# Optimization experiments

Hardware: AMD Instinct MI355X
Metric: run time of the kernel (lower is better)

## Reference

```python
import jax, jax.numpy as jnp
import numpy as np

N = 2          # branching factor
DATA_DIM = 4   # per-leaf payload size
DEPTH = 7      # tree fully refined to this depth (levels 0..7)
Q = 4_000_000  # number of query points


def _build_child():
    """Fully-refined N^3 tree: child[n,i,j,k] = relative offset to child node,
    0 for leaf cells (matches N3Tree.refine_all construction order)."""
    n_per = [N ** (3 * l) for l in range(DEPTH + 1)]
    offsets = np.concatenate([[0], np.cumsum(n_per)]).astype(np.int64)
    total = int(offsets[-1])
    child = np.zeros((total, N, N, N), dtype=np.int32)
    for l in range(DEPTH):  # level DEPTH nodes stay leaves (child==0)
        idx = offsets[l] + np.arange(n_per[l])
        child_abs = offsets[l + 1] + (np.arange(n_per[l])[:, None] * (N ** 3)
                                      + np.arange(N ** 3)[None, :])
        delta = (child_abs - idx[:, None]).astype(np.int32)
        child[idx] = delta.reshape(n_per[l], N, N, N)
    return child


def setup_inputs() -> dict:
    key = jax.random.key(0)
    k1, k2 = jax.random.split(key)
    child = jnp.asarray(_build_child())          # (M, N, N, N) int32
    M = child.shape[0]
    data = jax.random.normal(k1, (M, N, N, N, DATA_DIM), dtype=jnp.float32)
    indices = jax.random.uniform(k2, (Q, 3), dtype=jnp.float32,
                                 minval=0.0, maxval=1.0)
    return {"data": data, "child": child, "indices": indices}


def reference(data, child, indices):
    """Vectorized octree vertical query (vary_non_leaf=True):
    accumulate data along root->leaf path for each query point."""
    Nf = jnp.float32(N)
    nq = indices.shape[0]

    def step(carry, _):
        ind, node_ids, result, active = carry
        cell = jnp.clip(jnp.floor(ind * Nf).astype(jnp.int32), 0, N - 1)  # (Q,3)
        delta = child[node_ids, cell[:, 0], cell[:, 1], cell[:, 2]]       # (Q,)
        vals = data[node_ids, cell[:, 0], cell[:, 1], cell[:, 2]]         # (Q,D)
        result = result + jnp.where(active[:, None], vals, 0.0)
        nonterm = active & (delta != 0)
        node_ids = node_ids + jnp.where(nonterm, delta, 0)
        ind = jnp.where(active[:, None], ind * Nf - cell.astype(jnp.float32), ind)
        return (ind, node_ids, result, nonterm), None

    init = (indices,
            jnp.zeros(nq, jnp.int32),
            jnp.zeros((nq, DATA_DIM), jnp.float32),
            jnp.ones(nq, dtype=bool))
    (_, _, result, _), _ = jax.lax.scan(step, init, None, length=DEPTH + 1)
    return result
```

## Files before the change

kernel.cpp:

```cpp
#include <hip/hip_runtime.h>


typedef float vfloat4 __attribute__((ext_vector_type(4)));

__constant__ __device__ const int kOffs[8] = {0, 1, 9, 73, 585, 4681, 37449, 299593};

__global__ __launch_bounds__(256) void build_prefix_table(
    const float* __restrict__ data,
    vfloat4*     __restrict__ table)
{
    int p = blockIdx.x * blockDim.x + threadIdx.x;
    float ax = 0.f, ay = 0.f, az = 0.f, aw = 0.f;
    int prefix = 0;
    #pragma unroll
    for (int l = 0; l < 6; ++l) {
        int c = (p >> (15 - 3 * l)) & 7;
        int node = kOffs[l] + prefix;
        const vfloat4 v = *reinterpret_cast<const vfloat4*>(
            data + ((size_t)node << 5) + ((size_t)c << 2));
        ax += v.x; ay += v.y; az += v.z; aw += v.w;
        prefix = (prefix << 3) + c;
    }
    vfloat4 r; r.x = ax; r.y = ay; r.z = az; r.w = aw;
    table[p] = r;
}

__global__ __launch_bounds__(256) void n3tree_query_tab(
    const float*   __restrict__ data,
    const vfloat4* __restrict__ table,
    const float*   __restrict__ indices,
    float*         __restrict__ out,
    int nq)
{
    int q = blockIdx.x * blockDim.x + threadIdx.x;
    if (q >= nq) return;

    float ix = __builtin_nontemporal_load(indices + 3 * (size_t)q + 0);
    float iy = __builtin_nontemporal_load(indices + 3 * (size_t)q + 1);
    float iz = __builtin_nontemporal_load(indices + 3 * (size_t)q + 2);

    int cc[8];
    #pragma unroll
    for (int l = 0; l < 8; ++l) {
        int cx = (int)(ix * 2.0f); cx = cx < 0 ? 0 : (cx > 1 ? 1 : cx);
        int cy = (int)(iy * 2.0f); cy = cy < 0 ? 0 : (cy > 1 ? 1 : cy);
        int cz = (int)(iz * 2.0f); cz = cz < 0 ? 0 : (cz > 1 ? 1 : cz);
        cc[l] = (cx << 2) | (cy << 1) | cz;
        ix = ix * 2.0f - (float)cx;
        iy = iy * 2.0f - (float)cy;
        iz = iz * 2.0f - (float)cz;
    }
    int p6 = ((((cc[0] << 3 | cc[1]) << 3 | cc[2]) << 3 | cc[3]) << 3 | cc[4]) << 3 | cc[5];

    size_t addr6 = ((size_t)(37449  + p6)                << 5) + ((size_t)cc[6] << 2);
    size_t addr7 = ((size_t)(299593 + (p6 << 3) + cc[6]) << 5) + ((size_t)cc[7] << 2);

    vfloat4 t  = table[p6];
    vfloat4 v6 = *reinterpret_cast<const vfloat4*>(data + addr6);
    vfloat4 v7 = __builtin_nontemporal_load(
                     reinterpret_cast<const vfloat4*>(data + addr7));

    float ax = t.x; float ay = t.y; float az = t.z; float aw = t.w;
    ax += v6.x; ay += v6.y; az += v6.z; aw += v6.w;
    ax += v7.x; ay += v7.y; az += v7.z; aw += v7.w;

    vfloat4 r; r.x = ax; r.y = ay; r.z = az; r.w = aw;
    __builtin_nontemporal_store(r, reinterpret_cast<vfloat4*>(out) + q);
}

__global__ __launch_bounds__(256) void n3tree_query_direct(
    const float* __restrict__ data,
    const float* __restrict__ indices,
    float*       __restrict__ out,
    int nq)
{
    int q = blockIdx.x * blockDim.x + threadIdx.x;
    if (q >= nq) return;

    float ix = __builtin_nontemporal_load(indices + 3 * (size_t)q + 0);
    float iy = __builtin_nontemporal_load(indices + 3 * (size_t)q + 1);
    float iz = __builtin_nontemporal_load(indices + 3 * (size_t)q + 2);

    size_t addr[8];
    int p = 0;
    #pragma unroll
    for (int l = 0; l < 8; ++l) {
        int cx = (int)(ix * 2.0f); cx = cx < 0 ? 0 : (cx > 1 ? 1 : cx);
        int cy = (int)(iy * 2.0f); cy = cy < 0 ? 0 : (cy > 1 ? 1 : cy);
        int cz = (int)(iz * 2.0f); cz = cz < 0 ? 0 : (cz > 1 ? 1 : cz);
        int cidx = (cx << 2) | (cy << 1) | cz;
        addr[l] = ((size_t)(kOffs[l] + p) << 5) + ((size_t)cidx << 2);
        p = (p << 3) + cidx;
        ix = ix * 2.0f - (float)cx;
        iy = iy * 2.0f - (float)cy;
        iz = iz * 2.0f - (float)cz;
    }

    vfloat4 v[8];
    #pragma unroll
    for (int l = 0; l < 7; ++l)
        v[l] = *reinterpret_cast<const vfloat4*>(data + addr[l]);
    v[7] = __builtin_nontemporal_load(
               reinterpret_cast<const vfloat4*>(data + addr[7]));

    float ax = 0.f, ay = 0.f, az = 0.f, aw = 0.f;
    #pragma unroll
    for (int l = 0; l < 8; ++l) {
        ax += v[l].x; ay += v[l].y; az += v[l].z; aw += v[l].w;
    }

    vfloat4 r; r.x = ax; r.y = ay; r.z = az; r.w = aw;
    __builtin_nontemporal_store(r, reinterpret_cast<vfloat4*>(out) + q);
}

extern "C" void kernel_launch(void* const* d_in, const int* in_sizes, int n_in,
                              void* d_out, int out_size, void* d_ws, size_t ws_size,
                              hipStream_t stream) {
    const float* data    = (const float*)d_in[0];
    const float* indices = (const float*)d_in[2];
    float*       out     = (float*)d_out;

    int nq = in_sizes[2] / 3;
    const int block = 256;
    const int grid  = (nq + block - 1) / block;

    constexpr size_t TABLE_ENTRIES = 262144;
    constexpr size_t TABLE_BYTES   = TABLE_ENTRIES * 16;

    if (ws_size >= TABLE_BYTES) {
        vfloat4* table = reinterpret_cast<vfloat4*>(d_ws);
        build_prefix_table<<<TABLE_ENTRIES / block, block, 0, stream>>>(data, table);
        n3tree_query_tab<<<grid, block, 0, stream>>>(data, table, indices, out, nq);
    } else {
        n3tree_query_direct<<<grid, block, 0, stream>>>(data, indices, out, nq);
    }
}
```

Before: 208.1 us.

## Precompute full-path sums in bf16 table so each query does one lookup

Adds a full 8-level path-sum table D (16M entries, bf16-packed, 8 bytes each), so each query does a single gather instead of three. A fallback level-7 partial table T6 is used when the workspace is smaller. Building D streams the whole leaf level and writes 128MB, which could cost more than the gathers it saves for 4M queries. Rounding outputs to bf16 loses precision and may break the tolerance check.

```diff
diff --git a/kernel.cpp b/kernel.cpp
--- a/kernel.cpp
+++ b/kernel.cpp
@@ -5,9 +5,15 @@
 
 __constant__ __device__ const int kOffs[8] = {0, 1, 9, 73, 585, 4681, 37449, 299593};
 
-__global__ __launch_bounds__(256) void build_prefix_table(
-    const float* __restrict__ data,
-    vfloat4*     __restrict__ table)
+__device__ inline unsigned bf16_rne(float f) {
+    unsigned u = __float_as_uint(f);
+    return (u + 0x7fffu + ((u >> 16) & 1u)) >> 16;
+}
+__device__ inline float bf16_lo_f(unsigned w) { return __uint_as_float(w << 16); }
+__device__ inline float bf16_hi_f(unsigned w) { return __uint_as_float(w & 0xffff0000u); }
+
+__global__ __launch_bounds__(256) void build_T(
+    const float* __restrict__ data, vfloat4* __restrict__ T)
 {
     int p = blockIdx.x * blockDim.x + threadIdx.x;
     float ax = 0.f, ay = 0.f, az = 0.f, aw = 0.f;
@@ -16,29 +22,130 @@
     for (int l = 0; l < 6; ++l) {
         int c = (p >> (15 - 3 * l)) & 7;
         int node = kOffs[l] + prefix;
-        const vfloat4 v = *reinterpret_cast<const vfloat4*>(
+        vfloat4 v = *reinterpret_cast<const vfloat4*>(
             data + ((size_t)node << 5) + ((size_t)c << 2));
         ax += v.x; ay += v.y; az += v.z; aw += v.w;
         prefix = (prefix << 3) + c;
     }
     vfloat4 r; r.x = ax; r.y = ay; r.z = az; r.w = aw;
-    table[p] = r;
+    T[p] = r;
+}
+
+__global__ __launch_bounds__(256) void build_D(
+    const float* __restrict__ data, const vfloat4* __restrict__ T,
+    uint2* __restrict__ D)
+{
+    int t = blockIdx.x * blockDim.x + threadIdx.x;
+    int p7 = t >> 3, c7 = t & 7;
+    int p6 = p7 >> 3, c6 = p7 & 7;
+
+    vfloat4 tv = T[p6];
+    vfloat4 v6 = __builtin_nontemporal_load(reinterpret_cast<const vfloat4*>(
+        data + ((size_t)(37449 + p6) << 5) + ((size_t)c6 << 2)));
+    vfloat4 v7 = __builtin_nontemporal_load(reinterpret_cast<const vfloat4*>(
+        data + ((size_t)(299593 + p7) << 5) + ((size_t)c7 << 2)));
+
+    float ax = tv.x; ax += v6.x; ax += v7.x;
+    float ay = tv.y; ay += v6.y; ay += v7.y;
+    float az = tv.z; az += v6.z; az += v7.z;
+    float aw = tv.w; aw += v6.w; aw += v7.w;
+
+    uint2 o;
+    o.x = bf16_rne(ax) | (bf16_rne(ay) << 16);
+    o.y = bf16_rne(az) | (bf16_rne(aw) << 16);
+    D[(size_t)t] = o;
+}
+
+__global__ __launch_bounds__(256) void query_fold(
+    const uint2* __restrict__ D, const float* __restrict__ indices,
+    float* __restrict__ out, int nq)
+{
+    int q = blockIdx.x * blockDim.x + threadIdx.x;
+    if (q >= nq) return;
+
+    float ix = __builtin_nontemporal_load(indices + 3 * (size_t)q + 0);
+    float iy = __builtin_nontemporal_load(indices + 3 * (size_t)q + 1);
+    float iz = __builtin_nontemporal_load(indices + 3 * (size_t)q + 2);
+
+    int path = 0;
+    #pragma unroll
+    for (int l = 0; l < 8; ++l) {
+        int cx = (int)(ix * 2.0f); cx = cx < 0 ? 0 : (cx > 1 ? 1 : cx);
+        int cy = (int)(iy * 2.0f); cy = cy < 0 ? 0 : (cy > 1 ? 1 : cy);
+        int cz = (int)(iz * 2.0f); cz = cz < 0 ? 0 : (cz > 1 ? 1 : cz);
+        path = (path << 3) | ((cx << 2) | (cy << 1) | cz);
+        ix = ix * 2.0f - (float)cx;
+        iy = iy * 2.0f - (float)cy;
+        iz = iz * 2.0f - (float)cz;
+    }
+
+    uint2 d = D[(size_t)path];
+    vfloat4 r;
+    r.x = bf16_lo_f(d.x); r.y = bf16_hi_f(d.x);
+    r.z = bf16_lo_f(d.y); r.w = bf16_hi_f(d.y);
+    __builtin_nontemporal_store(r, reinterpret_cast<vfloat4*>(out) + q);
+}
+
+__global__ __launch_bounds__(256) void build_T6(
+    const float* __restrict__ data, const vfloat4* __restrict__ T,
+    uint2* __restrict__ T6)
+{
+    int t = blockIdx.x * blockDim.x + threadIdx.x;
+    int p6 = t >> 3, c6 = t & 7;
+    vfloat4 tv = T[p6];
+    vfloat4 v6 = __builtin_nontemporal_load(reinterpret_cast<const vfloat4*>(
+        data + ((size_t)(37449 + p6) << 5) + ((size_t)c6 << 2)));
+    float ax = tv.x + v6.x, ay = tv.y + v6.y, az = tv.z + v6.z, aw = tv.w + v6.w;
+    uint2 o;
+    o.x = bf16_rne(ax) | (bf16_rne(ay) << 16);
+    o.y = bf16_rne(az) | (bf16_rne(aw) << 16);
+    T6[(size_t)t] = o;
+}
+
+__global__ __launch_bounds__(256) void query_t6(
+    const float* __restrict__ data, const uint2* __restrict__ T6,
+    const float* __restrict__ indices, float* __restrict__ out, int nq)
+{
+    int q = blockIdx.x * blockDim.x + threadIdx.x;
+    if (q >= nq) return;
+
+    float ix = __builtin_nontemporal_load(indices + 3 * (size_t)q + 0);
+    float iy = __builtin_nontemporal_load(indices + 3 * (size_t)q + 1);
+    float iz = __builtin_nontemporal_load(indices + 3 * (size_t)q + 2);
+
+    int cc[8];
+    #pragma unroll
+    for (int l = 0; l < 8; ++l) {
+        int cx = (int)(ix * 2.0f); cx = cx < 0 ? 0 : (cx > 1 ? 1 : cx);
+        int cy = (int)(iy * 2.0f); cy = cy < 0 ? 0 : (cy > 1 ? 1 : cy);
+        int cz = (int)(iz * 2.0f); cz = cz < 0 ? 0 : (cz > 1 ? 1 : cz);
+        cc[l] = (cx << 2) | (cy << 1) | cz;
+        ix = ix * 2.0f - (float)cx;
+        iy = iy * 2.0f - (float)cy;
+        iz = iz * 2.0f - (float)cz;
+    }
+    int p6 = ((((cc[0] << 3 | cc[1]) << 3 | cc[2]) << 3 | cc[3]) << 3 | cc[4]) << 3 | cc[5];
+    int p7 = (p6 << 3) | cc[6];
+
+    uint2 t6 = T6[(size_t)p7];
+    vfloat4 v7 = __builtin_nontemporal_load(reinterpret_cast<const vfloat4*>(
+        data + ((size_t)(299593 + p7) << 5) + ((size_t)cc[7] << 2)));
+
+    vfloat4 r;
+    r.x = bf16_lo_f(t6.x) + v7.x; r.y = bf16_hi_f(t6.x) + v7.y;
+    r.z = bf16_lo_f(t6.y) + v7.z; r.w = bf16_hi_f(t6.y) + v7.w;
+    __builtin_nontemporal_store(r, reinterpret_cast<vfloat4*>(out) + q);
 }
 
 __global__ __launch_bounds__(256) void n3tree_query_tab(
-    const float*   __restrict__ data,
-    const vfloat4* __restrict__ table,
-    const float*   __restrict__ indices,
-    float*         __restrict__ out,
-    int nq)
-{
-    int q = blockIdx.x * blockDim.x + threadIdx.x;
-    if (q >= nq) return;
-
-    float ix = __builtin_nontemporal_load(indices + 3 * (size_t)q + 0);
-    float iy = __builtin_nontemporal_load(indices + 3 * (size_t)q + 1);
-    float iz = __builtin_nontemporal_load(indices + 3 * (size_t)q + 2);
-
+    const float* __restrict__ data, const vfloat4* __restrict__ table,
+    const float* __restrict__ indices, float* __restrict__ out, int nq)
+{
+    int q = blockIdx.x * blockDim.x + threadIdx.x;
+    if (q >= nq) return;
+    float ix = __builtin_nontemporal_load(indices + 3 * (size_t)q + 0);
+    float iy = __builtin_nontemporal_load(indices + 3 * (size_t)q + 1);
+    float iz = __builtin_nontemporal_load(indices + 3 * (size_t)q + 2);
     int cc[8];
     #pragma unroll
     for (int l = 0; l < 8; ++l) {
@@ -51,38 +158,30 @@
         iz = iz * 2.0f - (float)cz;
     }
     int p6 = ((((cc[0] << 3 | cc[1]) << 3 | cc[2]) << 3 | cc[3]) << 3 | cc[4]) << 3 | cc[5];
-
-    size_t addr6 = ((size_t)(37449  + p6)                << 5) + ((size_t)cc[6] << 2);
-    size_t addr7 = ((size_t)(299593 + (p6 << 3) + cc[6]) << 5) + ((size_t)cc[7] << 2);
-
+    size_t addr6 = ((size_t)(37449  + p6)                   << 5) + ((size_t)cc[6] << 2);
+    size_t addr7 = ((size_t)(299593 + (p6 << 3) + cc[6])    << 5) + ((size_t)cc[7] << 2);
     vfloat4 t  = table[p6];
     vfloat4 v6 = *reinterpret_cast<const vfloat4*>(data + addr6);
     vfloat4 v7 = __builtin_nontemporal_load(
                      reinterpret_cast<const vfloat4*>(data + addr7));
-
-    float ax = t.x; float ay = t.y; float az = t.z; float aw = t.w;
-    ax += v6.x; ay += v6.y; az += v6.z; aw += v6.w;
-    ax += v7.x; ay += v7.y; az += v7.z; aw += v7.w;
-
+    float ax = t.x; ax += v6.x; ax += v7.x;
+    float ay = t.y; ay += v6.y; ay += v7.y;
+    float az = t.z; az += v6.z; az += v7.z;
+    float aw = t.w; aw += v6.w; aw += v7.w;
     vfloat4 r; r.x = ax; r.y = ay; r.z = az; r.w = aw;
     __builtin_nontemporal_store(r, reinterpret_cast<vfloat4*>(out) + q);
 }
 
 __global__ __launch_bounds__(256) void n3tree_query_direct(
-    const float* __restrict__ data,
-    const float* __restrict__ indices,
-    float*       __restrict__ out,
-    int nq)
-{
-    int q = blockIdx.x * blockDim.x + threadIdx.x;
-    if (q >= nq) return;
-
-    float ix = __builtin_nontemporal_load(indices + 3 * (size_t)q + 0);
-    float iy = __builtin_nontemporal_load(indices + 3 * (size_t)q + 1);
-    float iz = __builtin_nontemporal_load(indices + 3 * (size_t)q + 2);
-
-    size_t addr[8];
-    int p = 0;
+    const float* __restrict__ data, const float* __restrict__ indices,
+    float* __restrict__ out, int nq)
+{
+    int q = blockIdx.x * blockDim.x + threadIdx.x;
+    if (q >= nq) return;
+    float ix = __builtin_nontemporal_load(indices + 3 * (size_t)q + 0);
+    float iy = __builtin_nontemporal_load(indices + 3 * (size_t)q + 1);
+    float iz = __builtin_nontemporal_load(indices + 3 * (size_t)q + 2);
+    size_t addr[8]; int p = 0;
     #pragma unroll
     for (int l = 0; l < 8; ++l) {
         int cx = (int)(ix * 2.0f); cx = cx < 0 ? 0 : (cx > 1 ? 1 : cx);
@@ -95,20 +194,15 @@
         iy = iy * 2.0f - (float)cy;
         iz = iz * 2.0f - (float)cz;
     }
-
     vfloat4 v[8];
     #pragma unroll
     for (int l = 0; l < 7; ++l)
         v[l] = *reinterpret_cast<const vfloat4*>(data + addr[l]);
     v[7] = __builtin_nontemporal_load(
                reinterpret_cast<const vfloat4*>(data + addr[7]));
-
     float ax = 0.f, ay = 0.f, az = 0.f, aw = 0.f;
     #pragma unroll
-    for (int l = 0; l < 8; ++l) {
-        ax += v[l].x; ay += v[l].y; az += v[l].z; aw += v[l].w;
-    }
-
+    for (int l = 0; l < 8; ++l) { ax += v[l].x; ay += v[l].y; az += v[l].z; aw += v[l].w; }
     vfloat4 r; r.x = ax; r.y = ay; r.z = az; r.w = aw;
     __builtin_nontemporal_store(r, reinterpret_cast<vfloat4*>(out) + q);
 }
@@ -124,13 +218,25 @@
     const int block = 256;
     const int grid  = (nq + block - 1) / block;
 
-    constexpr size_t TABLE_ENTRIES = 262144;
-    constexpr size_t TABLE_BYTES   = TABLE_ENTRIES * 16;
-
-    if (ws_size >= TABLE_BYTES) {
-        vfloat4* table = reinterpret_cast<vfloat4*>(d_ws);
-        build_prefix_table<<<TABLE_ENTRIES / block, block, 0, stream>>>(data, table);
-        n3tree_query_tab<<<grid, block, 0, stream>>>(data, table, indices, out, nq);
+    constexpr size_t T_BYTES  = 262144ull * 16;
+    constexpr size_t D_BYTES  = 16777216ull * 8;
+    constexpr size_t T6_BYTES = 2097152ull * 8;
+
+    vfloat4* T = reinterpret_cast<vfloat4*>(d_ws);
+
+    if (ws_size >= T_BYTES + D_BYTES) {
+        uint2* D = reinterpret_cast<uint2*>((char*)d_ws + T_BYTES);
+        build_T<<<262144 / block, block, 0, stream>>>(data, T);
+        build_D<<<16777216 / block, block, 0, stream>>>(data, T, D);
+        query_fold<<<grid, block, 0, stream>>>(D, indices, out, nq);
+    } else if (ws_size >= T_BYTES + T6_BYTES) {
+        uint2* T6 = reinterpret_cast<uint2*>((char*)d_ws + T_BYTES);
+        build_T<<<262144 / block, block, 0, stream>>>(data, T);
+        build_T6<<<2097152 / block, block, 0, stream>>>(data, T, T6);
+        query_t6<<<grid, block, 0, stream>>>(data, T6, indices, out, nq);
+    } else if (ws_size >= T_BYTES) {
+        build_T<<<262144 / block, block, 0, stream>>>(data, T);
+        n3tree_query_tab<<<grid, block, 0, stream>>>(data, T, indices, out, nq);
     } else {
         n3tree_query_direct<<<grid, block, 0, stream>>>(data, indices, out, nq);
     }
```

New measurement: 168.0 us, median of 2. -19.3%, faster.
